# Kernel optimization log

Hardware: AMD Instinct MI355X
Metric: run time of the kernel (lower is better)

## Reference

```python
import jax, jax.numpy as jnp
import numpy as np

QLEN, MLEN, BSZ = 1024, 1024, 2
D_MODEL, H, D_HEAD, D_FF = 1024, 16, 64, 4096
KLEN = QLEN + MLEN


def _ln(x, g, b, eps=1e-5):
    mu = jnp.mean(x, axis=-1, keepdims=True)
    var = jnp.var(x, axis=-1, keepdims=True)
    return (x - mu) * jax.lax.rsqrt(var + eps) * g + b


def _rel_shift(x):
    # x: [q, k, b, n] -> Transformer-XL relative shift
    q, k, b, n = x.shape
    zp = jnp.zeros((q, 1, b, n), x.dtype)
    xp = jnp.concatenate([zp, x], axis=1).reshape(k + 1, q, b, n)[1:]
    return xp.reshape(q, k, b, n)


def setup_inputs() -> dict:
    key = jax.random.key(0)
    ks = jax.random.split(key, 12)
    s = 0.02
    inp = {
        "input_": jax.random.normal(ks[0], (QLEN, BSZ, D_MODEL), jnp.float32),
        "mems": jax.random.normal(ks[1], (MLEN, BSZ, D_MODEL), jnp.float32),
        "pos_emb": jax.random.normal(ks[2], (KLEN, 1, D_MODEL), jnp.float32),
        # True = masked. Causal with memory: query i sees keys j <= i + MLEN
        "mask_tgt": jnp.triu(jnp.ones((QLEN, KLEN), bool), k=MLEN + 1),
        "ln1_g": jnp.ones((D_MODEL,), jnp.float32),
        "ln1_b": jnp.zeros((D_MODEL,), jnp.float32),
        "qkv_w": jax.random.normal(ks[3], (D_MODEL, 3 * H * D_HEAD), jnp.float32) * s,
        "qkv_b": jnp.zeros((3 * H * D_HEAD,), jnp.float32),
        "r_w": jax.random.normal(ks[4], (D_MODEL, H * D_HEAD), jnp.float32) * s,
        "r_w_bias": jax.random.normal(ks[5], (H, D_HEAD), jnp.float32) * s,
        "r_r_bias": jax.random.normal(ks[6], (H, D_HEAD), jnp.float32) * s,
        "o_w": jax.random.normal(ks[7], (H * D_HEAD, D_MODEL), jnp.float32) * s,
        "ln2_g": jnp.ones((D_MODEL,), jnp.float32),
        "ln2_b": jnp.zeros((D_MODEL,), jnp.float32),
        "ff_w1": jax.random.normal(ks[8], (D_MODEL, D_FF), jnp.float32) * s,
        "ff_b1": jnp.zeros((D_FF,), jnp.float32),
        "ff_w2": jax.random.normal(ks[9], (D_FF, D_MODEL), jnp.float32) * s,
        "ff_b2": jnp.zeros((D_MODEL,), jnp.float32),
    }
    return inp


def reference(input_, mems, pos_emb, mask_tgt, ln1_g, ln1_b, qkv_w, qkv_b,
              r_w, r_w_bias, r_r_bias, o_w, ln2_g, ln2_b,
              ff_w1, ff_b1, ff_w2, ff_b2):
    qlen, bsz, _ = input_.shape
    # --- pre-norm (applied to both current input and mems) ---
    q_in = _ln(input_, ln1_g, ln1_b)
    m_in = _ln(mems, ln1_g, ln1_b)
    cat = jnp.concatenate([m_in, q_in], axis=0)            # [klen, b, d]
    klen = cat.shape[0]
    heads = cat @ qkv_w + qkv_b                            # [klen, b, 3*h*dh]
    w_q, w_k, w_v = jnp.split(heads, 3, axis=-1)
    w_q = w_q[-qlen:].reshape(qlen, bsz, H, D_HEAD)        # [q, b, h, dh]
    w_k = w_k.reshape(klen, bsz, H, D_HEAD)
    w_v = w_v.reshape(klen, bsz, H, D_HEAD)
    r_k = (pos_emb[:, 0] @ r_w).reshape(klen, H, D_HEAD)   # [k, h, dh]

    AC = jnp.einsum('ibnd,jbnd->ijbn', w_q + r_w_bias, w_k)
    BD = jnp.einsum('ibnd,jnd->ijbn', w_q + r_r_bias, r_k)
    BD = _rel_shift(BD)
    scale = 1.0 / np.sqrt(D_HEAD)
    score = (AC + BD) * scale                              # [q, k, b, h]
    score = jnp.where(mask_tgt[:, :, None, None], -1e30, score)
    prob = jax.nn.softmax(score, axis=1)
    attn = jnp.einsum('ijbn,jbnd->ibnd', prob, w_v).reshape(qlen, bsz, H * D_HEAD)
    attn_out = attn @ o_w                                  # [q, b, d]
    x = input_ + attn_out                                  # residual (dropout = eval)

    # --- FFN block ---
    y = _ln(x, ln2_g, ln2_b)
    y = jax.nn.relu(y @ ff_w1 + ff_b1) @ ff_w2 + ff_b2
    return x + y
```

## Files before the change

kernel.cpp:

```cpp
#include <hip/hip_runtime.h>


typedef unsigned short u16;
typedef unsigned int   u32;
typedef __attribute__((ext_vector_type(8))) short bf16x8;
typedef __attribute__((ext_vector_type(4))) float f32x4;

struct alignas(16) U128 { u32 x[4]; };
struct alignas(16) F128 { float f[4]; };
struct alignas(8)  U64  { u32 x[2]; };

#define DEV static __device__ __forceinline__
#define MF(a, b, c) __builtin_amdgcn_mfma_f32_16x16x32_bf16((a), (b), (c), 0, 0, 0)

typedef __attribute__((address_space(1))) u32 as1_u32;
typedef __attribute__((address_space(3))) u32 as3_u32;
DEV void gload16(const void* g, void* l) {
  __builtin_amdgcn_global_load_lds((as1_u32*)g, (as3_u32*)l, 16, 0, 0);
}

DEV u16 f2bf(float f) {
  union { float f; u32 u; } v; v.f = f;
  u32 r = v.u + 0x7fffu + ((v.u >> 16) & 1u);
  return (u16)(r >> 16);
}
DEV float bf2f(u16 h) {
  union { u32 u; float f; } v; v.u = ((u32)h) << 16;
  return v.f;
}

template <int TWO>
__global__ __launch_bounds__(256) void ln_rows(
    const float* __restrict__ src, const float* __restrict__ src2,
    const float* __restrict__ g, const float* __restrict__ b,
    u16* __restrict__ dst)
{
  int row = blockIdx.x, tid = threadIdx.x;
  const float* s_;
  if constexpr (TWO) s_ = (row < 2048) ? src + (size_t)row * 1024
                                       : src2 + (size_t)(row - 2048) * 1024;
  else s_ = src + (size_t)row * 1024;
  F128 v = ((const F128*)s_)[tid];
  float s = v.f[0] + v.f[1] + v.f[2] + v.f[3];
  float q = v.f[0]*v.f[0] + v.f[1]*v.f[1] + v.f[2]*v.f[2] + v.f[3]*v.f[3];
#pragma unroll
  for (int off = 1; off < 64; off <<= 1) {
    s += __shfl_xor(s, off); q += __shfl_xor(q, off);
  }
  __shared__ float sh[8];
  int wid = tid >> 6;
  if ((tid & 63) == 0) { sh[wid] = s; sh[4 + wid] = q; }
  __syncthreads();
  s = sh[0] + sh[1] + sh[2] + sh[3];
  q = sh[4] + sh[5] + sh[6] + sh[7];
  float mu = s * (1.0f / 1024.0f);
  float rs = rsqrtf(q * (1.0f / 1024.0f) - mu * mu + 1e-5f);
  F128 g4 = ((const F128*)g)[tid];
  F128 b4 = ((const F128*)b)[tid];
  union { u16 h[4]; U64 u; } o;
#pragma unroll
  for (int j = 0; j < 4; j++)
    o.h[j] = f2bf((v.f[j] - mu) * rs * g4.f[j] + b4.f[j]);
  *(U64*)(dst + (size_t)row * 1024 + tid * 4) = o.u;
}

__global__ __launch_bounds__(256) void ln_fuse(
    const u16* __restrict__ p0, const u16* __restrict__ p1,
    const float* __restrict__ resid, const float* __restrict__ g,
    const float* __restrict__ b, float* __restrict__ X, u16* __restrict__ YN)
{
  int row = blockIdx.x, tid = threadIdx.x;
  U64 a = ((const U64*)(p0 + (size_t)row * 1024))[tid];
  U64 c = ((const U64*)(p1 + (size_t)row * 1024))[tid];
  F128 rv = ((const F128*)(resid + (size_t)row * 1024))[tid];
  float x[4];
  x[0] = bf2f((u16)a.x[0]) + bf2f((u16)c.x[0]) + rv.f[0];
  x[1] = bf2f((u16)(a.x[0] >> 16)) + bf2f((u16)(c.x[0] >> 16)) + rv.f[1];
  x[2] = bf2f((u16)a.x[1]) + bf2f((u16)c.x[1]) + rv.f[2];
  x[3] = bf2f((u16)(a.x[1] >> 16)) + bf2f((u16)(c.x[1] >> 16)) + rv.f[3];
  F128 xo;
#pragma unroll
  for (int j = 0; j < 4; j++) xo.f[j] = x[j];
  *(F128*)(X + (size_t)row * 1024 + tid * 4) = xo;

  float s = x[0] + x[1] + x[2] + x[3];
  float q = x[0]*x[0] + x[1]*x[1] + x[2]*x[2] + x[3]*x[3];
#pragma unroll
  for (int off = 1; off < 64; off <<= 1) {
    s += __shfl_xor(s, off); q += __shfl_xor(q, off);
  }
  __shared__ float sh[8];
  int wid = tid >> 6;
  if ((tid & 63) == 0) { sh[wid] = s; sh[4 + wid] = q; }
  __syncthreads();
  s = sh[0] + sh[1] + sh[2] + sh[3];
  q = sh[4] + sh[5] + sh[6] + sh[7];
  float mu = s * (1.0f / 1024.0f);
  float rs = rsqrtf(q * (1.0f / 1024.0f) - mu * mu + 1e-5f);
  F128 g4 = ((const F128*)g)[tid];
  F128 b4 = ((const F128*)b)[tid];
  union { u16 h[4]; U64 u; } o;
#pragma unroll
  for (int j = 0; j < 4; j++)
    o.h[j] = f2bf((x[j] - mu) * rs * g4.f[j] + b4.f[j]);
  *(U64*)(YN + (size_t)row * 1024 + tid * 4) = o.u;
}

__global__ __launch_bounds__(256) void transpose_w(
    const float* __restrict__ W, u16* __restrict__ Wt, int K, int N)
{
  __shared__ float t[64][65];
  int k0 = blockIdx.x * 64, n0 = blockIdx.y * 64;
  int tid = threadIdx.x;
  int r = tid >> 6, c = tid & 63;
#pragma unroll
  for (int i = 0; i < 16; i++)
    t[r + i * 4][c] = W[(size_t)(k0 + r + i * 4) * N + n0 + c];
  __syncthreads();
#pragma unroll
  for (int i = 0; i < 16; i++) {
    int n = r + i * 4;
    Wt[(size_t)(n0 + n) * K + k0 + c] = f2bf(t[c][n]);
  }
}

__global__ __launch_bounds__(256) void cvt_bf16(
    const float* __restrict__ s, u16* __restrict__ d, int n4)
{
  int i = blockIdx.x * 256 + threadIdx.x;
  if (i >= n4) return;
  F128 v = ((const F128*)s)[i];
  union { u16 h[4]; U64 u; } o;
#pragma unroll
  for (int j = 0; j < 4; j++) o.h[j] = f2bf(v.f[j]);
  ((U64*)d)[i] = o.u;
}

template <int EPI, int NSPLIT>
__global__ __launch_bounds__(256, 2) void gemm_bt(
    const u16* __restrict__ A, const u16* __restrict__ Bt,
    u16* __restrict__ outb, const float* __restrict__ bias,
    u16* __restrict__ p0, u16* __restrict__ p1,
    u16* __restrict__ p2, u16* __restrict__ p3,
    int M, int N, int K)
{
  __shared__ u16 As[2][128 * 64];
  __shared__ u16 Bs[2][128 * 64];
  int tid = threadIdx.x;
  int m0 = blockIdx.x * 128, n0 = blockIdx.y * 128;
  int lane = tid & 63, wid = tid >> 6;
  int wr = wid >> 1, wc = wid & 1;
  f32x4 acc[4][4] = {};

  const int Kc = K / NSPLIT;
  const int kbase = (NSPLIT > 1) ? (int)blockIdx.z * Kc : 0;

  const int lrow = wid * 8 + (lane >> 3);
  const int lcol = (lane & 7) * 8;
  const u16* Ag = A  + (size_t)(m0 + lrow) * K + kbase + lcol;
  const u16* Bg = Bt + (size_t)(n0 + lrow) * K + kbase + lcol;

  auto stage = [&](int buf, int k0) {
#pragma unroll
    for (int i = 0; i < 4; i++) {
      gload16(Ag + (size_t)i * 32 * K + k0, &As[buf][(i * 4 + wid) * 512]);
      gload16(Bg + (size_t)i * 32 * K + k0, &Bs[buf][(i * 4 + wid) * 512]);
    }
  };

  stage(0, 0);
  __syncthreads();
  int cur = 0;
  for (int k0 = 0; k0 < Kc; k0 += 64) {
    if (k0 + 64 < Kc) stage(cur ^ 1, k0 + 64);
    bf16x8 af[2][4], bfr[2][4];
#pragma unroll
    for (int kc = 0; kc < 2; kc++)
#pragma unroll
      for (int f = 0; f < 4; f++) {
        af[kc][f]  = *(const bf16x8*)&As[cur][(wr * 64 + f * 16 + (lane & 15)) * 64 + kc * 32 + (lane >> 4) * 8];
        bfr[kc][f] = *(const bf16x8*)&Bs[cur][(wc * 64 + f * 16 + (lane & 15)) * 64 + kc * 32 + (lane >> 4) * 8];
      }
    __builtin_amdgcn_s_setprio(1);
#pragma unroll
    for (int kc = 0; kc < 2; kc++)
#pragma unroll
      for (int fi = 0; fi < 4; fi++)
#pragma unroll
        for (int fj = 0; fj < 4; fj++)
          acc[fi][fj] = MF(af[kc][fi], bfr[kc][fj], acc[fi][fj]);
    __builtin_amdgcn_s_setprio(0);
    __syncthreads();
    cur ^= 1;
  }

  u16* part = nullptr;
  if constexpr (NSPLIT > 1) {
    part = (blockIdx.z == 0) ? p0 : (blockIdx.z == 1) ? p1
         : (blockIdx.z == 2) ? p2 : p3;
  }
#pragma unroll
  for (int fi = 0; fi < 4; fi++)
#pragma unroll
    for (int fj = 0; fj < 4; fj++) {
      int col = n0 + wc * 64 + fj * 16 + (lane & 15);
      float bvv = (NSPLIT == 1 && bias != nullptr) ? bias[col] : 0.0f;
#pragma unroll
      for (int r = 0; r < 4; r++) {
        int row = m0 + wr * 64 + fi * 16 + (lane >> 4) * 4 + r;
        float v = acc[fi][fj][r] + bvv;
        if constexpr (NSPLIT > 1) {
          part[(size_t)row * N + col] = f2bf(v);
        } else {
          if constexpr (EPI == 1) v = fmaxf(v, 0.0f);
          outb[(size_t)row * N + col] = f2bf(v);
        }
      }
    }
}

template <int NS, int EPI>
__global__ __launch_bounds__(256) void reduce_splitb(
    const u16* __restrict__ p0, const u16* __restrict__ p1,
    const u16* __restrict__ p2, const u16* __restrict__ p3,
    const float* __restrict__ bias, const float* __restrict__ resid,
    u16* __restrict__ outb, float* __restrict__ outf, int N)
{
  int e = (blockIdx.x * 256 + threadIdx.x) * 8;
  U128 a = *(const U128*)(p0 + e);
  U128 c = *(const U128*)(p1 + e);
  float v[8];
#pragma unroll
  for (int k = 0; k < 4; k++) {
    v[2*k]   = bf2f((u16)a.x[k]) + bf2f((u16)c.x[k]);
    v[2*k+1] = bf2f((u16)(a.x[k] >> 16)) + bf2f((u16)(c.x[k] >> 16));
  }
  if constexpr (NS == 4) {
    U128 d2 = *(const U128*)(p2 + e);
    U128 d3 = *(const U128*)(p3 + e);
#pragma unroll
    for (int k = 0; k < 4; k++) {
      v[2*k]   += bf2f((u16)d2.x[k]) + bf2f((u16)d3.x[k]);
      v[2*k+1] += bf2f((u16)(d2.x[k] >> 16)) + bf2f((u16)(d3.x[k] >> 16));
    }
  }
  if constexpr (EPI == 2) {
    F128 r0 = *(const F128*)(resid + e);
    F128 r1 = *(const F128*)(resid + e + 4);
    int col = e % N;
    F128 o0, o1;
#pragma unroll
    for (int j = 0; j < 4; j++) {
      float b0 = (bias != nullptr) ? bias[col + j] : 0.0f;
      float b1 = (bias != nullptr) ? bias[col + 4 + j] : 0.0f;
      o0.f[j] = v[j] + b0 + r0.f[j];
      o1.f[j] = v[4 + j] + b1 + r1.f[j];
    }
    *(F128*)(outf + e) = o0;
    *(F128*)(outf + e + 4) = o1;
  } else {
    U128 o;
#pragma unroll
    for (int k = 0; k < 4; k++)
      o.x[k] = (u32)f2bf(v[2*k]) | ((u32)f2bf(v[2*k+1]) << 16);
    *(U128*)(outb + e) = o;
  }
}

__global__ __launch_bounds__(256) void extract_vt(
    const u16* __restrict__ heads, u16* __restrict__ Vt)
{
  __shared__ u16 t[64][72];
  int jt = blockIdx.x;
  int bh = blockIdx.y;
  int b = bh >> 4, h = bh & 15;
  int tid = threadIdx.x;
  int row = tid >> 2;
  int cc = (tid & 3) * 16;
#pragma unroll
  for (int i = 0; i < 2; i++)
    *(U128*)&t[row][cc + i * 8] =
        *(const U128*)&heads[(size_t)((jt * 64 + row) * 2 + b) * 3072 + 2048 + h * 64 + cc + i * 8];
  __syncthreads();
  int jc = tid & 63, dr = tid >> 6;
#pragma unroll
  for (int i = 0; i < 16; i++) {
    int d = dr + i * 4;
    Vt[((size_t)bh * 64 + d) * 2048 + jt * 64 + jc] = t[jc][d];
  }
}

__global__ __launch_bounds__(256, 2) void attn_fwd(
    const u16* __restrict__ heads, const u16* __restrict__ rk,
    const u16* __restrict__ Vt, const float* __restrict__ rwb,
    const float* __restrict__ rrb, u16* __restrict__ attnout)
{
  __shared__ u16 lds[37376];

  int tid = threadIdx.x, lane = tid & 63, wid = tid >> 6;
  int bh = blockIdx.x;
  int y = (int)blockIdx.y;
  int xt = (y < 8) ? y : 23 - y;
  int i0 = xt * 64;
  int b = bh >> 4, h = bh & 15;
  const float SCL = 0.18033688f;

  u16* Ps = lds + 32768;
  u16* Qw = lds;
  u16* Qr = lds + 4608;

  for (int c = tid; c < 512; c += 256) {
    int row = c >> 3, c8 = (c & 7) * 8;
    union { U128 v; u16 h[8]; } in, ow, orr;
    in.v = *(const U128*)&heads[(size_t)((1024 + i0 + row) * 2 + b) * 3072 + h * 64 + c8];
#pragma unroll
    for (int j = 0; j < 8; j++) {
      float q = bf2f(in.h[j]);
      ow.h[j]  = f2bf(q + rwb[h * 64 + c8 + j]);
      orr.h[j] = f2bf(q + rrb[h * 64 + c8 + j]);
    }
    *(U128*)&Qw[row * 72 + c8] = ow.v;
    *(U128*)&Qr[row * 72 + c8] = orr.v;
  }
  __syncthreads();

  bf16x8 qwf[2], qrf[2];
  int qrow = wid * 16 + (lane & 15);
#pragma unroll
  for (int kc = 0; kc < 2; kc++) {
    qwf[kc] = *(const bf16x8*)&Qw[qrow * 72 + kc * 32 + (lane >> 4) * 8];
    qrf[kc] = *(const bf16x8*)&Qr[qrow * 72 + kc * 32 + (lane >> 4) * 8];
  }
  __syncthreads();

  const int srow = lane >> 3;
  const int scol = 8 * ((lane & 7) ^ srow);

  auto stage = [&](int buf, int t) {
    int j0 = t * 64;
    u16* base = lds + buf * 16384;
#pragma unroll
    for (int i = 0; i < 2; i++) {
      int g8 = wid * 2 + i;
      int jr = j0 + g8 * 8 + srow;
      gload16(heads + (size_t)(jr * 2 + b) * 3072 + 1024 + h * 64 + scol,
              base + g8 * 512);
    }
#pragma unroll
    for (int i = 0; i < 2; i++) {
      int g8 = wid * 2 + i;
      int dr = g8 * 8 + srow;
      gload16(Vt + ((size_t)bh * 64 + dr) * 2048 + j0 + scol,
              base + 4096 + g8 * 512);
    }
    int rbase = 960 + j0 - i0;
#pragma unroll
    for (int i = 0; i < 4; i++) {
      int g8 = wid * 4 + i;
      int rr = rbase + g8 * 8 + srow;
      rr = rr < 0 ? 0 : (rr > 2047 ? 2047 : rr);
      gload16(rk + (size_t)rr * 1024 + h * 64 + scol,
              base + 8192 + g8 * 512);
    }
  };

  stage(0, 0);
  __syncthreads();

  float mrow[4], plrow[4];
  f32x4 o[4] = {};
  f32x4 bd[5];
#pragma unroll
  for (int r = 0; r < 4; r++) { mrow[r] = -1e30f; plrow[r] = 0.0f; }

  int nt = i0 / 64 + 17;
  const int roffw = 48 - wid * 16;
  const int g = lane >> 4, cc = lane & 15;
  const int rswz = 8 * (lane & 7);

  for (int t = 0; t < nt; t++) {
    const u16* base = lds + (t & 1) * 16384;
    if (t + 1 < nt) stage((t + 1) & 1, t + 1);

    const u16* Kb = base;
    const u16* Vb = base + 4096;
    const u16* Rb = base + 8192;

    f32x4 sAC[4] = {};
    if (t == 0) bd[0] = (f32x4){0.f, 0.f, 0.f, 0.f};
#pragma unroll
    for (int fb = 1; fb < 5; fb++) bd[fb] = (f32x4){0.f, 0.f, 0.f, 0.f};
    __builtin_amdgcn_s_setprio(1);
#pragma unroll
    for (int kc = 0; kc < 2; kc++) {
      int cb = (kc * 32 + g * 8) ^ rswz;
#pragma unroll
      for (int fj = 0; fj < 4; fj++) {
        bf16x8 kf = *(const bf16x8*)&Kb[(fj * 16 + (lane & 15)) * 64 + cb];
        sAC[fj] = MF(qwf[kc], kf, sAC[fj]);
      }
      if (t == 0) {
        bf16x8 rf = *(const bf16x8*)&Rb[(roffw + (lane & 15)) * 64 + cb];
        bd[0] = MF(qrf[kc], rf, bd[0]);
      }
#pragma unroll
      for (int fb = 1; fb < 5; fb++) {
        bf16x8 rf = *(const bf16x8*)&Rb[(roffw + fb * 16 + (lane & 15)) * 64 + cb];
        bd[fb] = MF(qrf[kc], rf, bd[fb]);
      }
    }
    __builtin_amdgcn_s_setprio(0);

    float p[4][4];
#pragma unroll
    for (int fj = 0; fj < 4; fj++)
#pragma unroll
      for (int r = 0; r < 4; r++) {
        int sh_ = 15 - 4 * g - r;
        int src = (lane & 48) | ((lane + sh_) & 15);
        float lo = __shfl(bd[fj][r], src);
        float hi = __shfl(bd[fj + 1][r], src);
        float bdv = (cc + sh_ < 16) ? lo : hi;
        p[fj][r] = (sAC[fj][r] + bdv) * SCL;
      }
    bd[0] = bd[4];

    if (t == nt - 1) {
#pragma unroll
      for (int fj = 0; fj < 4; fj++)
#pragma unroll
        for (int r = 0; r < 4; r++)
          if (fj * 16 + cc > 16 * wid + 4 * g + r) p[fj][r] = -1e30f;
    }

    float tmax[4];
#pragma unroll
    for (int r = 0; r < 4; r++)
      tmax[r] = fmaxf(fmaxf(p[0][r], p[1][r]), fmaxf(p[2][r], p[3][r]));

    bool ok = true;
#pragma unroll
    for (int r = 0; r < 4; r++) ok &= (tmax[r] <= mrow[r] + 12.0f);
    if (!__all(ok)) {
#pragma unroll
      for (int off = 1; off < 16; off <<= 1)
#pragma unroll
        for (int r = 0; r < 4; r++)
          tmax[r] = fmaxf(tmax[r], __shfl_xor(tmax[r], off));
#pragma unroll
      for (int r = 0; r < 4; r++) {
        float mn = fmaxf(mrow[r], tmax[r]);
        float ms = exp2f(mrow[r] - mn);
        mrow[r] = mn;
        plrow[r] *= ms;
#pragma unroll
        for (int fd = 0; fd < 4; fd++) o[fd][r] *= ms;
      }
    }

#pragma unroll
    for (int fj = 0; fj < 4; fj++)
#pragma unroll
      for (int r = 0; r < 4; r++) {
        float e = exp2f(p[fj][r] - mrow[r]);
        plrow[r] += e;
        Ps[(wid * 16 + (lane >> 4) * 4 + r) * 72 + fj * 16 + (lane & 15)] = f2bf(e);
      }
    __builtin_amdgcn_s_setprio(1);
#pragma unroll
    for (int kc = 0; kc < 2; kc++) {
      bf16x8 pf = *(const bf16x8*)&Ps[(wid * 16 + (lane & 15)) * 72 + kc * 32 + g * 8];
      int cb = (kc * 32 + g * 8) ^ rswz;
#pragma unroll
      for (int fd = 0; fd < 4; fd++) {
        bf16x8 vf = *(const bf16x8*)&Vb[(fd * 16 + (lane & 15)) * 64 + cb];
        o[fd] = MF(pf, vf, o[fd]);
      }
    }
    __builtin_amdgcn_s_setprio(0);

    __syncthreads();
  }

#pragma unroll
  for (int off = 1; off < 16; off <<= 1)
#pragma unroll
    for (int r = 0; r < 4; r++)
      plrow[r] += __shfl_xor(plrow[r], off);
#pragma unroll
  for (int fd = 0; fd < 4; fd++)
#pragma unroll
    for (int r = 0; r < 4; r++) {
      int ii2 = (lane >> 4) * 4 + r;
      int row = (i0 + wid * 16 + ii2) * 2 + b;
      attnout[(size_t)row * 1024 + h * 64 + fd * 16 + (lane & 15)] = f2bf(o[fd][r] / plrow[r]);
    }
}

extern "C" void kernel_launch(void* const* d_in, const int* in_sizes, int n_in,
                              void* d_out, int out_size, void* d_ws, size_t ws_size,
                              hipStream_t stream)
{
  const float* input_ = (const float*)d_in[0];
  const float* mems   = (const float*)d_in[1];
  const float* pos    = (const float*)d_in[2];
  const float* ln1g = (const float*)d_in[4];
  const float* ln1b = (const float*)d_in[5];
  const float* qkvw = (const float*)d_in[6];
  const float* qkvb = (const float*)d_in[7];
  const float* rw   = (const float*)d_in[8];
  const float* rwb  = (const float*)d_in[9];
  const float* rrb  = (const float*)d_in[10];
  const float* ow   = (const float*)d_in[11];
  const float* ln2g = (const float*)d_in[12];
  const float* ln2b = (const float*)d_in[13];
  const float* fw1  = (const float*)d_in[14];
  const float* fb1  = (const float*)d_in[15];
  const float* fw2  = (const float*)d_in[16];
  const float* fb2  = (const float*)d_in[17];
  float* out = (float*)d_out;

  char* w = (char*)d_ws;
  u16* WT_QKV = (u16*)(w + 0);
  u16* WT_R   = (u16*)(w + 6291456);
  u16* WT_O   = (u16*)(w + 8388608);
  u16* WT_F1  = (u16*)(w + 10485760);
  u16* WT_F2  = (u16*)(w + 18874368);
  u16* POSB   = (u16*)(w + 27262976);
  u16* ATTN   = POSB;
  u16* CATLN  = (u16*)(w + 31457280);
  u16* HEADS  = (u16*)(w + 39845888);
  u16* H1     = HEADS;
  float* X    = (float*)(w + 56623104);
  u16* RK     = (u16*)(w + 65011712);
  u16* VT     = (u16*)(w + 69206016);
  u16* YN     = VT;

  u16* RKP0 = (u16*)(w + 31457280);
  u16* RKP1 = (u16*)(w + 69206016);
  u16* OWP0 = (u16*)(w + 39845888);
  u16* OWP1 = (u16*)(w + 44040192);
  u16* F2P0 = (u16*)(w + 0);
  u16* F2P1 = (u16*)(w + 10485760);
  u16* F2P2 = (u16*)(w + 31457280);
  u16* F2P3 = (u16*)(w + 65011712);

  dim3 blk(256);

  transpose_w<<<dim3(16, 48), blk, 0, stream>>>(qkvw, WT_QKV, 1024, 3072);
  transpose_w<<<dim3(16, 16), blk, 0, stream>>>(rw,   WT_R,   1024, 1024);
  transpose_w<<<dim3(16, 16), blk, 0, stream>>>(ow,   WT_O,   1024, 1024);
  transpose_w<<<dim3(16, 64), blk, 0, stream>>>(fw1,  WT_F1,  1024, 4096);
  transpose_w<<<dim3(64, 16), blk, 0, stream>>>(fw2,  WT_F2,  4096, 1024);
  cvt_bf16<<<dim3(2048), blk, 0, stream>>>(pos, POSB, 2048 * 1024 / 4);

  ln_rows<1><<<dim3(4096), blk, 0, stream>>>(mems, input_, ln1g, ln1b, CATLN);

  gemm_bt<0, 1><<<dim3(32, 24), blk, 0, stream>>>(
      CATLN, WT_QKV, HEADS, qkvb, nullptr, nullptr, nullptr, nullptr, 4096, 3072, 1024);
  gemm_bt<0, 2><<<dim3(16, 8, 2), blk, 0, stream>>>(
      POSB, WT_R, nullptr, nullptr, RKP0, RKP1, nullptr, nullptr, 2048, 1024, 1024);
  reduce_splitb<2, 0><<<dim3(1024), blk, 0, stream>>>(
      RKP0, RKP1, nullptr, nullptr, nullptr, nullptr, RK, nullptr, 1024);

  extract_vt<<<dim3(32, 32), blk, 0, stream>>>(HEADS, VT);
  attn_fwd<<<dim3(32, 16), blk, 0, stream>>>(HEADS, RK, VT, rwb, rrb, ATTN);

  gemm_bt<0, 2><<<dim3(16, 8, 2), blk, 0, stream>>>(
      ATTN, WT_O, nullptr, nullptr, OWP0, OWP1, nullptr, nullptr, 2048, 1024, 1024);
  ln_fuse<<<dim3(2048), blk, 0, stream>>>(OWP0, OWP1, input_, ln2g, ln2b, X, YN);

  gemm_bt<1, 1><<<dim3(16, 32), blk, 0, stream>>>(
      YN, WT_F1, H1, fb1, nullptr, nullptr, nullptr, nullptr, 2048, 4096, 1024);
  gemm_bt<0, 4><<<dim3(16, 8, 4), blk, 0, stream>>>(
      H1, WT_F2, nullptr, nullptr, F2P0, F2P1, F2P2, F2P3, 2048, 1024, 4096);
  reduce_splitb<4, 2><<<dim3(1024), blk, 0, stream>>>(
      F2P0, F2P1, F2P2, F2P3, fb2, X, nullptr, out, 1024);
}
```

Measured before the change: 231.8 us.

## Merge weight-prep launches, raise split-K to four for r and o GEMMs

Replaces the five transpose launches and the pos-embedding bf16 conversion with a single prep kernel that maps block ids onto the separate jobs, cutting launch overhead and filling the GPU at once. Raises split-K from 2 to 4 for the positional projection and output projection GEMMs, giving more blocks on a K=1024 problem; the reduce and ln_fuse kernels now read four partial buffers. The attention kernel's relative-shift code now shuffles each of the five BD fragments once per row instead of twice per column pair. The trade-off is more partial-buffer traffic in bf16, plus extra rounding from the additional bf16 partial sums.

```diff
diff --git a/kernel.cpp b/kernel.cpp
--- a/kernel.cpp
+++ b/kernel.cpp
@@ -66,18 +66,22 @@
 
 __global__ __launch_bounds__(256) void ln_fuse(
     const u16* __restrict__ p0, const u16* __restrict__ p1,
+    const u16* __restrict__ p2, const u16* __restrict__ p3,
     const float* __restrict__ resid, const float* __restrict__ g,
     const float* __restrict__ b, float* __restrict__ X, u16* __restrict__ YN)
 {
   int row = blockIdx.x, tid = threadIdx.x;
   U64 a = ((const U64*)(p0 + (size_t)row * 1024))[tid];
   U64 c = ((const U64*)(p1 + (size_t)row * 1024))[tid];
+  U64 d = ((const U64*)(p2 + (size_t)row * 1024))[tid];
+  U64 e = ((const U64*)(p3 + (size_t)row * 1024))[tid];
   F128 rv = ((const F128*)(resid + (size_t)row * 1024))[tid];
   float x[4];
-  x[0] = bf2f((u16)a.x[0]) + bf2f((u16)c.x[0]) + rv.f[0];
-  x[1] = bf2f((u16)(a.x[0] >> 16)) + bf2f((u16)(c.x[0] >> 16)) + rv.f[1];
-  x[2] = bf2f((u16)a.x[1]) + bf2f((u16)c.x[1]) + rv.f[2];
-  x[3] = bf2f((u16)(a.x[1] >> 16)) + bf2f((u16)(c.x[1] >> 16)) + rv.f[3];
+#pragma unroll
+  for (int k = 0; k < 2; k++) {
+    x[2*k]   = bf2f((u16)a.x[k]) + bf2f((u16)c.x[k]) + bf2f((u16)d.x[k]) + bf2f((u16)e.x[k]) + rv.f[2*k];
+    x[2*k+1] = bf2f((u16)(a.x[k] >> 16)) + bf2f((u16)(c.x[k] >> 16)) + bf2f((u16)(d.x[k] >> 16)) + bf2f((u16)(e.x[k] >> 16)) + rv.f[2*k+1];
+  }
   F128 xo;
 #pragma unroll
   for (int j = 0; j < 4; j++) xo.f[j] = x[j];
@@ -106,12 +110,32 @@
   *(U64*)(YN + (size_t)row * 1024 + tid * 4) = o.u;
 }
 
-__global__ __launch_bounds__(256) void transpose_w(
-    const float* __restrict__ W, u16* __restrict__ Wt, int K, int N)
-{
+__global__ __launch_bounds__(256) void prep_weights(
+    const float* __restrict__ qkvw, const float* __restrict__ rw,
+    const float* __restrict__ oww, const float* __restrict__ fw1,
+    const float* __restrict__ fw2, const float* __restrict__ pos,
+    u16* __restrict__ WT_QKV, u16* __restrict__ WT_R, u16* __restrict__ WT_O,
+    u16* __restrict__ WT_F1, u16* __restrict__ WT_F2, u16* __restrict__ POSB)
+{
+  int id = blockIdx.x, tid = threadIdx.x;
+  if (id >= 3328) {
+    int i = (id - 3328) * 256 + tid;
+    F128 v = ((const F128*)pos)[i];
+    union { u16 h[4]; U64 u; } o;
+#pragma unroll
+    for (int j = 0; j < 4; j++) o.h[j] = f2bf(v.f[j]);
+    ((U64*)POSB)[i] = o.u;
+    return;
+  }
+  const float* W; u16* Wt; int K, N, rem;
+  if (id < 768)       { W = qkvw; Wt = WT_QKV; K = 1024; N = 3072; rem = id; }
+  else if (id < 1024) { W = rw;   Wt = WT_R;   K = 1024; N = 1024; rem = id - 768; }
+  else if (id < 1280) { W = oww;  Wt = WT_O;   K = 1024; N = 1024; rem = id - 1024; }
+  else if (id < 2304) { W = fw1;  Wt = WT_F1;  K = 1024; N = 4096; rem = id - 1280; }
+  else                { W = fw2;  Wt = WT_F2;  K = 4096; N = 1024; rem = id - 2304; }
+  int nn = N >> 6;
+  int k0 = (rem / nn) * 64, n0 = (rem % nn) * 64;
   __shared__ float t[64][65];
-  int k0 = blockIdx.x * 64, n0 = blockIdx.y * 64;
-  int tid = threadIdx.x;
   int r = tid >> 6, c = tid & 63;
 #pragma unroll
   for (int i = 0; i < 16; i++)
@@ -122,18 +146,6 @@
     int n = r + i * 4;
     Wt[(size_t)(n0 + n) * K + k0 + c] = f2bf(t[c][n]);
   }
-}
-
-__global__ __launch_bounds__(256) void cvt_bf16(
-    const float* __restrict__ s, u16* __restrict__ d, int n4)
-{
-  int i = blockIdx.x * 256 + threadIdx.x;
-  if (i >= n4) return;
-  F128 v = ((const F128*)s)[i];
-  union { u16 h[4]; U64 u; } o;
-#pragma unroll
-  for (int j = 0; j < 4; j++) o.h[j] = f2bf(v.f[j]);
-  ((U64*)d)[i] = o.u;
 }
 
 template <int EPI, int NSPLIT>
@@ -413,16 +425,17 @@
 
     float p[4][4];
 #pragma unroll
-    for (int fj = 0; fj < 4; fj++)
-#pragma unroll
-      for (int r = 0; r < 4; r++) {
-        int sh_ = 15 - 4 * g - r;
-        int src = (lane & 48) | ((lane + sh_) & 15);
-        float lo = __shfl(bd[fj][r], src);
-        float hi = __shfl(bd[fj + 1][r], src);
-        float bdv = (cc + sh_ < 16) ? lo : hi;
-        p[fj][r] = (sAC[fj][r] + bdv) * SCL;
-      }
+    for (int r = 0; r < 4; r++) {
+      int sh_ = 15 - 4 * g - r;
+      int src = (lane & 48) | ((lane + sh_) & 15);
+      float rt[5];
+#pragma unroll
+      for (int fb = 0; fb < 5; fb++) rt[fb] = __shfl(bd[fb][r], src);
+      bool lo = (cc + sh_ < 16);
+#pragma unroll
+      for (int fj = 0; fj < 4; fj++)
+        p[fj][r] = (sAC[fj][r] + (lo ? rt[fj] : rt[fj + 1])) * SCL;
+    }
     bd[0] = bd[4];
 
     if (t == nt - 1) {
@@ -537,9 +550,13 @@
   u16* YN     = VT;
 
   u16* RKP0 = (u16*)(w + 31457280);
-  u16* RKP1 = (u16*)(w + 69206016);
+  u16* RKP1 = (u16*)(w + 35651584);
+  u16* RKP2 = (u16*)(w + 69206016);
+  u16* RKP3 = (u16*)(w + 73400320);
   u16* OWP0 = (u16*)(w + 39845888);
   u16* OWP1 = (u16*)(w + 44040192);
+  u16* OWP2 = (u16*)(w + 48234496);
+  u16* OWP3 = (u16*)(w + 52428800);
   u16* F2P0 = (u16*)(w + 0);
   u16* F2P1 = (u16*)(w + 10485760);
   u16* F2P2 = (u16*)(w + 31457280);
@@ -547,28 +564,25 @@
 
   dim3 blk(256);
 
-  transpose_w<<<dim3(16, 48), blk, 0, stream>>>(qkvw, WT_QKV, 1024, 3072);
-  transpose_w<<<dim3(16, 16), blk, 0, stream>>>(rw,   WT_R,   1024, 1024);
-  transpose_w<<<dim3(16, 16), blk, 0, stream>>>(ow,   WT_O,   1024, 1024);
-  transpose_w<<<dim3(16, 64), blk, 0, stream>>>(fw1,  WT_F1,  1024, 4096);
-  transpose_w<<<dim3(64, 16), blk, 0, stream>>>(fw2,  WT_F2,  4096, 1024);
-  cvt_bf16<<<dim3(2048), blk, 0, stream>>>(pos, POSB, 2048 * 1024 / 4);
+  prep_weights<<<dim3(5376), blk, 0, stream>>>(
+      qkvw, rw, ow, fw1, fw2, pos, WT_QKV, WT_R, WT_O, WT_F1, WT_F2, POSB);
 
   ln_rows<1><<<dim3(4096), blk, 0, stream>>>(mems, input_, ln1g, ln1b, CATLN);
 
   gemm_bt<0, 1><<<dim3(32, 24), blk, 0, stream>>>(
       CATLN, WT_QKV, HEADS, qkvb, nullptr, nullptr, nullptr, nullptr, 4096, 3072, 1024);
-  gemm_bt<0, 2><<<dim3(16, 8, 2), blk, 0, stream>>>(
-      POSB, WT_R, nullptr, nullptr, RKP0, RKP1, nullptr, nullptr, 2048, 1024, 1024);
-  reduce_splitb<2, 0><<<dim3(1024), blk, 0, stream>>>(
-      RKP0, RKP1, nullptr, nullptr, nullptr, nullptr, RK, nullptr, 1024);
+  gemm_bt<0, 4><<<dim3(16, 8, 4), blk, 0, stream>>>(
+      POSB, WT_R, nullptr, nullptr, RKP0, RKP1, RKP2, RKP3, 2048, 1024, 1024);
+  reduce_splitb<4, 0><<<dim3(1024), blk, 0, stream>>>(
+      RKP0, RKP1, RKP2, RKP3, nullptr, nullptr, RK, nullptr, 1024);
 
   extract_vt<<<dim3(32, 32), blk, 0, stream>>>(HEADS, VT);
   attn_fwd<<<dim3(32, 16), blk, 0, stream>>>(HEADS, RK, VT, rwb, rrb, ATTN);
 
-  gemm_bt<0, 2><<<dim3(16, 8, 2), blk, 0, stream>>>(
-      ATTN, WT_O, nullptr, nullptr, OWP0, OWP1, nullptr, nullptr, 2048, 1024, 1024);
-  ln_fuse<<<dim3(2048), blk, 0, stream>>>(OWP0, OWP1, input_, ln2g, ln2b, X, YN);
+  gemm_bt<0, 4><<<dim3(16, 8, 4), blk, 0, stream>>>(
+      ATTN, WT_O, nullptr, nullptr, OWP0, OWP1, OWP2, OWP3, 2048, 1024, 1024);
+  ln_fuse<<<dim3(2048), blk, 0, stream>>>(
+      OWP0, OWP1, OWP2, OWP3, input_, ln2g, ln2b, X, YN);
 
   gemm_bt<1, 1><<<dim3(16, 32), blk, 0, stream>>>(
       YN, WT_F1, H1, fb1, nullptr, nullptr, nullptr, nullptr, 2048, 4096, 1024);
```

Measured after the change: 259.3 us. 11.9% more time.
